# Performance work log

Hardware: AMD Instinct MI355X
Metric: run time of the kernel (lower is better)

## Reference

```python
import jax, jax.numpy as jnp
import numpy as np

B, S, D, L, V, H, FF = 128, 256, 512, 4, 96, 8, 512
DH = D // H
EPS = 1e-3  # keras BatchNormalization default epsilon


def setup_inputs() -> dict:
    key = jax.random.key(0)
    ks = jax.random.split(key, 12)
    s = 0.02
    inp = {
        "sequence": jax.random.randint(ks[0], (B, S), 0, V),
        "pos_encodings": jax.random.normal(ks[1], (S, D), jnp.float32) * s,
        "embed": jax.random.normal(ks[2], (V, D), jnp.float32) * s,
        "Wq": jax.random.normal(ks[3], (L, D, D), jnp.float32) * s,
        "bq": jnp.zeros((L, D), jnp.float32),
        "Wk": jax.random.normal(ks[4], (L, D, D), jnp.float32) * s,
        "bk": jnp.zeros((L, D), jnp.float32),
        "Wv": jax.random.normal(ks[5], (L, D, D), jnp.float32) * s,
        "bv": jnp.zeros((L, D), jnp.float32),
        "Wo": jax.random.normal(ks[6], (L, D, D), jnp.float32) * s,
        "bo": jnp.zeros((L, D), jnp.float32),
        "gamma1": jnp.ones((L, D), jnp.float32),
        "beta1": jnp.zeros((L, D), jnp.float32),
        "W1": jax.random.normal(ks[7], (L, D, FF), jnp.float32) * s,
        "b1": jnp.zeros((L, FF), jnp.float32),
        "W2": jax.random.normal(ks[8], (L, FF, D), jnp.float32) * s,
        "b2": jnp.zeros((L, D), jnp.float32),
        "gamma2": jnp.ones((L, D), jnp.float32),
        "beta2": jnp.zeros((L, D), jnp.float32),
    }
    return inp


def _batchnorm(h, g, b):
    # training-mode BN over (batch, seq) per feature, eps=1e-3
    mu = jnp.mean(h, axis=(0, 1), keepdims=True)
    var = jnp.mean(jnp.square(h - mu), axis=(0, 1), keepdims=True)
    return (h - mu) * jax.lax.rsqrt(var + EPS) * g + b


def _encoder(sequence, pos_encodings, embed, layer_params):
    x = embed[sequence] + pos_encodings[None]  # [B,S,D]

    def layer(h, p):
        wq, bq_, wk, bk_, wv, bv_, wo, bo_, g1, be1, w1, bb1, w2, bb2, g2, be2 = p
        b_, s_, d_ = h.shape
        q = (h @ wq + bq_).reshape(b_, s_, H, DH)
        k = (h @ wk + bk_).reshape(b_, s_, H, DH)
        v = (h @ wv + bv_).reshape(b_, s_, H, DH)
        scores = jnp.einsum('bqhd,bkhd->bhqk', q, k) / jnp.sqrt(jnp.float32(DH))
        attn = jnp.einsum('bhqk,bkhd->bqhd', jax.nn.softmax(scores, axis=-1), v)
        attn = attn.reshape(b_, s_, d_) @ wo + bo_
        h = _batchnorm(h + attn, g1, be1)
        ffn = jax.nn.relu(h @ w1 + bb1) @ w2 + bb2
        h = _batchnorm(h + ffn, g2, be2)
        return h, None

    out, _ = jax.lax.scan(layer, x, layer_params)
    return out


def reference(sequence, pos_encodings, embed, Wq, bq, Wk, bk, Wv, bv, Wo, bo,
              gamma1, beta1, W1, b1, W2, b2, gamma2, beta2):
    layer_params = (Wq, bq, Wk, bk, Wv, bv, Wo, bo,
                    gamma1, beta1, W1, b1, W2, b2, gamma2, beta2)
    return _encoder(sequence, pos_encodings, embed, layer_params)
```

## Files before the change

### kernel.cpp

```cpp
#include <hip/hip_runtime.h>

#define B_   128
#define S_   256
#define D_   512
#define L_   4
#define H_   8
#define DH_  64
#define FF_  512
#define M_   32768
#define EPS_ 1e-3f

typedef unsigned short u16;
typedef unsigned int   u32;
typedef __bf16 bf16_8 __attribute__((ext_vector_type(8)));
typedef float  f32_4  __attribute__((ext_vector_type(4)));

__device__ __forceinline__ float bf2f(u16 u) {
  union { u32 i; float f; } x; x.i = ((u32)u) << 16; return x.f;
}
__device__ __forceinline__ u16 f2bf(float f) {
  union { float f; u32 i; } x; x.f = f;
  u32 r = x.i + 0x7fffu + ((x.i >> 16) & 1u);
  return (u16)(r >> 16);
}
__device__ __forceinline__ void async_cp16(const void* g, void* l) {
  __builtin_amdgcn_global_load_lds(
      (const __attribute__((address_space(1))) void*)g,
      (__attribute__((address_space(3))) void*)l, 16, 0, 0);
}

__global__ __launch_bounds__(256) void k_embed(const int* __restrict__ seq,
    const float* __restrict__ pos, const float* __restrict__ emb,
    u16* __restrict__ h)
{
  int t = blockIdx.x * 256 + threadIdx.x;
  int row = t >> 6;
  int c = (t & 63) * 8;
  int s = row & (S_ - 1);
  int tok = seq[row];
  const float* ep = emb + (size_t)tok * D_ + c;
  const float* pp = pos + (size_t)s * D_ + c;
  float4 e0 = *(const float4*)ep;
  float4 e1 = *(const float4*)(ep + 4);
  float4 p0 = *(const float4*)pp;
  float4 p1 = *(const float4*)(pp + 4);
  u32 o[4];
  o[0] = (u32)f2bf(e0.x + p0.x) | ((u32)f2bf(e0.y + p0.y) << 16);
  o[1] = (u32)f2bf(e0.z + p0.z) | ((u32)f2bf(e0.w + p0.w) << 16);
  o[2] = (u32)f2bf(e1.x + p1.x) | ((u32)f2bf(e1.y + p1.y) << 16);
  o[3] = (u32)f2bf(e1.z + p1.z) | ((u32)f2bf(e1.w + p1.w) << 16);
  *(uint4*)&h[(size_t)row * D_ + c] = make_uint4(o[0], o[1], o[2], o[3]);
}

__global__ __launch_bounds__(256) void k_transpose(
    const float* __restrict__ Wq, const float* __restrict__ Wk, const float* __restrict__ Wv,
    const float* __restrict__ Wo, const float* __restrict__ W1, const float* __restrict__ W2,
    u16* __restrict__ Wt)
{
  __shared__ u16 tile[32][33];
  int mat = blockIdx.z;
  int layer = mat / 6, w = mat % 6;
  const float* src = (w == 0) ? Wq : (w == 1) ? Wk : (w == 2) ? Wv
                   : (w == 3) ? Wo : (w == 4) ? W1 : W2;
  src += (size_t)layer * (D_ * D_);
  u16* dst = Wt + (size_t)mat * (D_ * D_);
  int bx = blockIdx.x * 32;
  int by = blockIdx.y * 32;
  int tx = threadIdx.x & 31, ty = threadIdx.x >> 5;
#pragma unroll
  for (int i = 0; i < 32; i += 8)
    tile[ty + i][tx] = f2bf(src[(size_t)(by + ty + i) * D_ + bx + tx]);
  __syncthreads();
#pragma unroll
  for (int i = 0; i < 32; i += 8)
    dst[(size_t)(bx + ty + i) * D_ + by + tx] = tile[tx][ty + i];
}

__global__ __launch_bounds__(256) void k_packbias(const float* __restrict__ bq,
    const float* __restrict__ bk, const float* __restrict__ bv, float* __restrict__ dst)
{
  int t = blockIdx.x * 256 + threadIdx.x;
  int l = t / 1536, j = t - l * 1536;
  const float* src = (j < 512) ? bq : (j < 1024) ? bk : bv;
  dst[t] = src[l * 512 + (j & 511)];
}

__global__ __launch_bounds__(256) void k_gemm(
    const u16* __restrict__ A, const u16* __restrict__ Bt,
    const float* __restrict__ bias, const u16* __restrict__ resid,
    u16* __restrict__ outb, float* __restrict__ stats,
    int mode)
{
  __shared__ __align__(16) u16 smem[24576];
  u16* As = smem;
  u16* Bs = smem + 12288;
  int tid = threadIdx.x;
  int m0 = blockIdx.x * 128;
  int n0 = blockIdx.y * 128;
  int w = tid >> 6, lane = tid & 63;
  int wm = (w >> 1) * 64, wn = (w & 1) * 64;
  int fr = lane & 15, lk = lane >> 4;

  int srow = lane >> 2;
  int schunk = (lane & 3) ^ ((lane >> 4) & 3);
  const u16* Ag0 = A  + (size_t)(m0 + w * 32 + srow) * 512 + schunk * 8;
  const u16* Ag1 = Ag0 + (size_t)16 * 512;
  const u16* Bg0 = Bt + (size_t)(n0 + w * 32 + srow) * 512 + schunk * 8;
  const u16* Bg1 = Bg0 + (size_t)16 * 512;
  int off0 = (w * 32) * 32;
  int off1 = (w * 32 + 16) * 32;

  f32_4 acc[4][4] = {};
  int ach = (lk ^ ((fr >> 2) & 3)) * 8;

  async_cp16(Ag0, &As[off0]);
  async_cp16(Ag1, &As[off1]);
  async_cp16(Bg0, &Bs[off0]);
  async_cp16(Bg1, &Bs[off1]);
  async_cp16(Ag0 + 32, &As[4096 + off0]);
  async_cp16(Ag1 + 32, &As[4096 + off1]);
  async_cp16(Bg0 + 32, &Bs[4096 + off0]);
  async_cp16(Bg1 + 32, &Bs[4096 + off1]);

#pragma unroll
  for (int it = 0; it < 16; it++) {
    if (it < 15) asm volatile("s_waitcnt vmcnt(4)" ::: "memory");
    else         asm volatile("s_waitcnt vmcnt(0)" ::: "memory");
    __builtin_amdgcn_s_barrier();
    asm volatile("" ::: "memory");
    if (it < 14) {
      int kn = (it + 2) * 32;
      int pn = ((it + 2) % 3) * 4096;
      async_cp16(Ag0 + kn, &As[pn + off0]);
      async_cp16(Ag1 + kn, &As[pn + off1]);
      async_cp16(Bg0 + kn, &Bs[pn + off0]);
      async_cp16(Bg1 + kn, &Bs[pn + off1]);
    }
    const u16* Ab = &As[(it % 3) * 4096];
    const u16* Bb = &Bs[(it % 3) * 4096];
    bf16_8 afr[4], bfr[4];
#pragma unroll
    for (int i = 0; i < 4; i++) {
      afr[i] = *(const bf16_8*)&Ab[(wm + i * 16 + fr) * 32 + ach];
      bfr[i] = *(const bf16_8*)&Bb[(wn + i * 16 + fr) * 32 + ach];
    }
#pragma unroll
    for (int i = 0; i < 4; i++)
#pragma unroll
      for (int j = 0; j < 4; j++)
        acc[i][j] = __builtin_amdgcn_mfma_f32_16x16x32_bf16(afr[i], bfr[j], acc[i][j], 0, 0, 0);
  }

  __syncthreads();
  u16* Ct = smem;
  int rbase = lk * 4;
#pragma unroll
  for (int j = 0; j < 4; j++) {
    int colin = wn + j * 16 + fr;
    int colg  = n0 + colin;
    float bv = bias[colg];
    float csum = 0.f, csq = 0.f;
#pragma unroll
    for (int i = 0; i < 4; i++) {
      int rowl = wm + i * 16 + rbase;
#pragma unroll
      for (int r = 0; r < 4; r++) {
        float c = acc[i][j][r] + bv;
        if (mode == 1) c = fmaxf(c, 0.f);
        if (mode == 2) {
          c += bf2f(resid[(size_t)(m0 + rowl + r) * 512 + colg]);
          csum += c; csq = fmaf(c, c, csq);
        }
        int rw = rowl + r;
        Ct[rw * 128 + (((colin >> 3) ^ (rw & 15)) << 3) + (colin & 7)] = f2bf(c);
      }
    }
    if (mode == 2) {
      csum += __shfl_xor(csum, 16); csum += __shfl_xor(csum, 32);
      csq  += __shfl_xor(csq, 16);  csq  += __shfl_xor(csq, 32);
      if (lk == 0) {
        atomicAdd(&stats[colg], csum);
        atomicAdd(&stats[512 + colg], csq);
      }
    }
  }
  __syncthreads();

#pragma unroll
  for (int rd = 0; rd < 8; rd++) {
    int lrow = w * 32 + rd * 4 + (lane >> 4);
    int s = lane & 15;
    uint4 val = *(const uint4*)&Ct[lrow * 128 + s * 8];
    int chunk = s ^ (lrow & 15);
    int grow = m0 + lrow;
    if (mode == 3) {
      int colg = n0 + chunk * 8;
      int cc = colg & 511;
      size_t idx = (size_t)(colg >> 9) * ((size_t)M_ * D_)
                 + ((size_t)((grow >> 8) * 8 + (cc >> 6)) * 256 + (grow & 255)) * 64 + (cc & 63);
      *(uint4*)&outb[idx] = val;
    } else {
      *(uint4*)&outb[(size_t)grow * 512 + n0 + chunk * 8] = val;
    }
  }
}

__global__ __launch_bounds__(256) void k_attn(
    const u16* __restrict__ q, const u16* __restrict__ k,
    const u16* __restrict__ v, u16* __restrict__ attn)
{
  __shared__ u16 Vt[64 * 256];
  __shared__ u16 Pm[4][16 * 64];
  int tid = threadIdx.x;
  int h = blockIdx.x & 7, b = blockIdx.x >> 3;
  size_t hb = (size_t)(b * 8 + h) * (256 * 64);
  int w = tid >> 6, lane = tid & 63;

  {
    int kp = tid & 127;
    int o  = tid >> 7;
    const u16* vp = v + hb + (size_t)(2 * kp) * 64 + o * 32;
    union { uint4 u[4]; u16 s[32]; } r0, r1;
#pragma unroll
    for (int i = 0; i < 4; i++) {
      r0.u[i] = *(const uint4*)(vp + i * 8);
      r1.u[i] = *(const uint4*)(vp + 64 + i * 8);
    }
#pragma unroll
    for (int d = 0; d < 32; d++) {
      int da = o * 32 + d;
      u32 val = (u32)r0.s[d] | ((u32)r1.s[d] << 16);
      int idx = da * 256 + ((((kp >> 2) ^ (da & 31)) << 3)) + ((2 * kp) & 7);
      *(u32*)&Vt[idx] = val;
    }
  }
  __syncthreads();

  int fr = lane & 15;
  int lk = lane >> 4;
  int rbase = lk * 4;
  const u16* kb = k + hb;

#pragma unroll 1
  for (int qt = 0; qt < 4; qt++) {
    int q0 = qt * 64 + w * 16;

    f32_4 accS[16];
    const u16* qbase = q + hb + (size_t)(q0 + fr) * 64 + lk * 8;
    bf16_8 af0 = *(const bf16_8*)(qbase);
    bf16_8 af1 = *(const bf16_8*)(qbase + 32);
#pragma unroll
    for (int j = 0; j < 16; j++) {
      const u16* kr = kb + (size_t)(j * 16 + fr) * 64;
      bf16_8 bf0 = *(const bf16_8*)(kr + lk * 8);
      bf16_8 bf1 = *(const bf16_8*)(kr + 32 + lk * 8);
      f32_4 z = {};
      z = __builtin_amdgcn_mfma_f32_16x16x32_bf16(af0, bf0, z, 0, 0, 0);
      accS[j] = __builtin_amdgcn_mfma_f32_16x16x32_bf16(af1, bf1, z, 0, 0, 0);
    }

    float l[4];
#pragma unroll
    for (int r = 0; r < 4; r++) {
      float m = accS[0][r];
#pragma unroll
      for (int j = 1; j < 16; j++) m = fmaxf(m, accS[j][r]);
      m = fmaxf(m, __shfl_xor(m, 1));
      m = fmaxf(m, __shfl_xor(m, 2));
      m = fmaxf(m, __shfl_xor(m, 4));
      m = fmaxf(m, __shfl_xor(m, 8));
      float s = 0.f;
#pragma unroll
      for (int j = 0; j < 16; j++) {
        float p = __expf((accS[j][r] - m) * 0.125f);
        accS[j][r] = p;
        s += p;
      }
      s += __shfl_xor(s, 1);
      s += __shfl_xor(s, 2);
      s += __shfl_xor(s, 4);
      s += __shfl_xor(s, 8);
      l[r] = s;
    }

    f32_4 accO[4] = {};
#pragma unroll
    for (int hs = 0; hs < 4; hs++) {
#pragma unroll
      for (int j4 = 0; j4 < 4; j4++) {
        int col = j4 * 16 + fr;
        int ch = col >> 3, cl = col & 7;
#pragma unroll
        for (int r = 0; r < 4; r++) {
          int row = rbase + r;
          Pm[w][row * 64 + ((ch ^ (row & 7)) << 3) + cl] = f2bf(accS[hs * 4 + j4][r]);
        }
      }
#pragma unroll
      for (int kk = 0; kk < 2; kk++) {
        bf16_8 pa = *(const bf16_8*)&Pm[w][fr * 64 + (((kk * 4 + lk) ^ (fr & 7)) << 3)];
#pragma unroll
        for (int jd = 0; jd < 4; jd++) {
          int brow = jd * 16 + fr;
          int ck = hs * 8 + kk * 4 + lk;
          bf16_8 vb = *(const bf16_8*)&Vt[brow * 256 + ((ck ^ (brow & 31)) << 3)];
          accO[jd] = __builtin_amdgcn_mfma_f32_16x16x32_bf16(pa, vb, accO[jd], 0, 0, 0);
        }
      }
    }

    float linv[4];
#pragma unroll
    for (int r = 0; r < 4; r++) linv[r] = 1.f / l[r];
    size_t orow0 = (size_t)(b * S_ + q0 + rbase);
#pragma unroll
    for (int jd = 0; jd < 4; jd++) {
      int col = h * DH_ + jd * 16 + fr;
#pragma unroll
      for (int r = 0; r < 4; r++)
        attn[(orow0 + r) * D_ + col] = f2bf(accO[jd][r] * linv[r]);
    }
  }
}

__global__ __launch_bounds__(256) void k_zero(float* p, int n) {
  int t = blockIdx.x * 256 + threadIdx.x;
  if (t < n) p[t] = 0.f;
}

__global__ __launch_bounds__(256) void k_bnapply(const u16* __restrict__ P,
    const float* __restrict__ stats, const float* __restrict__ gamma,
    const float* __restrict__ beta, u16* __restrict__ outb, float* __restrict__ outf)
{
  size_t t8 = ((size_t)blockIdx.x * 256 + threadIdx.x) * 8;
  int f = (int)(t8 & 511);
  const float inv = 1.f / 32768.f;
  float sc[8], sh[8];
#pragma unroll
  for (int i = 0; i < 8; i++) {
    float mu = stats[f + i] * inv;
    float var = stats[512 + f + i] * inv - mu * mu;
    sc[i] = gamma[f + i] * rsqrtf(var + EPS_);
    sh[i] = beta[f + i] - mu * sc[i];
  }
  union { uint4 u; u16 s[8]; } pv;
  pv.u = *(const uint4*)&P[t8];
  float o[8];
#pragma unroll
  for (int i = 0; i < 8; i++) o[i] = bf2f(pv.s[i]) * sc[i] + sh[i];
  if (outf) {
    *(float4*)&outf[t8]     = make_float4(o[0], o[1], o[2], o[3]);
    *(float4*)&outf[t8 + 4] = make_float4(o[4], o[5], o[6], o[7]);
  } else {
    u32 u[4];
#pragma unroll
    for (int i = 0; i < 4; i++)
      u[i] = (u32)f2bf(o[2 * i]) | ((u32)f2bf(o[2 * i + 1]) << 16);
    *(uint4*)&outb[t8] = make_uint4(u[0], u[1], u[2], u[3]);
  }
}

extern "C" void kernel_launch(void* const* d_in, const int* in_sizes, int n_in,
                              void* d_out, int out_size, void* d_ws, size_t ws_size,
                              hipStream_t stream)
{
  const int*   seq = (const int*)d_in[0];
  const float* pos = (const float*)d_in[1];
  const float* emb = (const float*)d_in[2];
  const float* Wq  = (const float*)d_in[3];
  const float* bq  = (const float*)d_in[4];
  const float* Wk  = (const float*)d_in[5];
  const float* bk  = (const float*)d_in[6];
  const float* Wv  = (const float*)d_in[7];
  const float* bv  = (const float*)d_in[8];
  const float* Wo  = (const float*)d_in[9];
  const float* bo  = (const float*)d_in[10];
  const float* g1  = (const float*)d_in[11];
  const float* be1 = (const float*)d_in[12];
  const float* W1  = (const float*)d_in[13];
  const float* b1  = (const float*)d_in[14];
  const float* W2  = (const float*)d_in[15];
  const float* b2  = (const float*)d_in[16];
  const float* g2  = (const float*)d_in[17];
  const float* be2 = (const float*)d_in[18];

  char* ws = (char*)d_ws;
  const size_t SZH = (size_t)M_ * D_ * 2;
  u16* hb16 = (u16*)(ws);
  u16* qB   = (u16*)(ws + SZH);
  u16* kB   = (u16*)(ws + 2 * SZH);
  u16* vB   = (u16*)(ws + 3 * SZH);
  u16* aB   = (u16*)(ws + 4 * SZH);
  u16* PB   = (u16*)(ws + 2 * SZH);
  u16* tB   = qB;
  u16* Wt   = (u16*)(ws + 5 * SZH);
  float* stats = (float*)(ws + 5 * SZH + (size_t)24 * D_ * D_ * 2);
  float* bqkv  = stats + 8192;

  dim3 blk(256);
  k_zero<<<32, blk, 0, stream>>>(stats, 8192);
  k_packbias<<<24, blk, 0, stream>>>(bq, bk, bv, bqkv);
  k_transpose<<<dim3(16, 16, 24), blk, 0, stream>>>(Wq, Wk, Wv, Wo, W1, W2, Wt);
  k_embed<<<M_ * 64 / 256, blk, 0, stream>>>(seq, pos, emb, hb16);

  dim3 ggrid(M_ / 128, 512 / 128);
  dim3 qgrid(M_ / 128, 1536 / 128);
  for (int l = 0; l < L_; l++) {
    const u16* wtqkv = Wt + (size_t)(l * 6 + 0) * D_ * D_;
    const u16* wto = Wt + (size_t)(l * 6 + 3) * D_ * D_;
    const u16* wt1 = Wt + (size_t)(l * 6 + 4) * D_ * D_;
    const u16* wt2 = Wt + (size_t)(l * 6 + 5) * D_ * D_;
    float* st = stats + l * 2048;

    k_gemm<<<qgrid, blk, 0, stream>>>(hb16, wtqkv, bqkv + l * 1536, nullptr, qB, nullptr, 3);
    k_attn<<<B_ * H_, blk, 0, stream>>>(qB, kB, vB, aB);
    k_gemm<<<ggrid, blk, 0, stream>>>(aB, wto, bo + l * D_, hb16, PB, st, 2);
    k_bnapply<<<8192, blk, 0, stream>>>(PB, st, g1 + l * D_, be1 + l * D_, hb16, nullptr);
    k_gemm<<<ggrid, blk, 0, stream>>>(hb16, wt1, b1 + l * FF_, nullptr, tB, nullptr, 1);
    k_gemm<<<ggrid, blk, 0, stream>>>(tB, wt2, b2 + l * D_, hb16, PB, st + 1024, 2);
    if (l == L_ - 1)
      k_bnapply<<<8192, blk, 0, stream>>>(PB, st + 1024, g2 + l * D_, be2 + l * D_, nullptr, (float*)d_out);
    else
      k_bnapply<<<8192, blk, 0, stream>>>(PB, st + 1024, g2 + l * D_, be2 + l * D_, hb16, nullptr);
  }
}
```

Baseline: 1.561 ms.

## Recompute attention scores in two passes and swap GEMM grid order

The attention kernel no longer keeps all 16 score tiles in registers. A first pass computes QK^T only to get the row max, and a second pass recomputes the scores chunk by chunk, exponentiating and feeding P·V straight away. This cuts register pressure to allow more waves per CU, at the cost of computing QK^T twice. Separately, the GEMM grid now puts the N tiles on blockIdx.x, so blocks that share the same A rows launch next to each other and can reuse them in L2.

Measured after the change: 1.681 ms. 1.08x slower.

```diff
diff --git a/kernel.cpp b/kernel.cpp
--- a/kernel.cpp
+++ b/kernel.cpp
@@ -95,8 +95,8 @@
   u16* As = smem;
   u16* Bs = smem + 12288;
   int tid = threadIdx.x;
-  int m0 = blockIdx.x * 128;
-  int n0 = blockIdx.y * 128;
+  int m0 = blockIdx.y * 128;
+  int n0 = blockIdx.x * 128;
   int w = tid >> 6, lane = tid & 63;
   int wm = (w >> 1) * 64, wn = (w & 1) * 64;
   int fr = lane & 15, lk = lane >> 4;
@@ -244,74 +244,90 @@
 #pragma unroll 1
   for (int qt = 0; qt < 4; qt++) {
     int q0 = qt * 64 + w * 16;
-
-    f32_4 accS[16];
     const u16* qbase = q + hb + (size_t)(q0 + fr) * 64 + lk * 8;
     bf16_8 af0 = *(const bf16_8*)(qbase);
     bf16_8 af1 = *(const bf16_8*)(qbase + 32);
-#pragma unroll
+
+    float mrow[4] = {-1e30f, -1e30f, -1e30f, -1e30f};
+#pragma unroll 4
     for (int j = 0; j < 16; j++) {
       const u16* kr = kb + (size_t)(j * 16 + fr) * 64;
       bf16_8 bf0 = *(const bf16_8*)(kr + lk * 8);
       bf16_8 bf1 = *(const bf16_8*)(kr + 32 + lk * 8);
       f32_4 z = {};
       z = __builtin_amdgcn_mfma_f32_16x16x32_bf16(af0, bf0, z, 0, 0, 0);
-      accS[j] = __builtin_amdgcn_mfma_f32_16x16x32_bf16(af1, bf1, z, 0, 0, 0);
-    }
-
-    float l[4];
+      z = __builtin_amdgcn_mfma_f32_16x16x32_bf16(af1, bf1, z, 0, 0, 0);
+      mrow[0] = fmaxf(mrow[0], z[0]);
+      mrow[1] = fmaxf(mrow[1], z[1]);
+      mrow[2] = fmaxf(mrow[2], z[2]);
+      mrow[3] = fmaxf(mrow[3], z[3]);
+    }
 #pragma unroll
     for (int r = 0; r < 4; r++) {
-      float m = accS[0][r];
-#pragma unroll
-      for (int j = 1; j < 16; j++) m = fmaxf(m, accS[j][r]);
+      float m = mrow[r];
       m = fmaxf(m, __shfl_xor(m, 1));
       m = fmaxf(m, __shfl_xor(m, 2));
       m = fmaxf(m, __shfl_xor(m, 4));
       m = fmaxf(m, __shfl_xor(m, 8));
-      float s = 0.f;
-#pragma unroll
-      for (int j = 0; j < 16; j++) {
-        float p = __expf((accS[j][r] - m) * 0.125f);
-        accS[j][r] = p;
-        s += p;
-      }
+      mrow[r] = m;
+    }
+
+    float lrow[4] = {0.f, 0.f, 0.f, 0.f};
+    f32_4 accO[4] = {};
+#pragma unroll 1
+    for (int qq = 0; qq < 4; qq++) {
+      f32_4 accS4[4];
+#pragma unroll
+      for (int j4 = 0; j4 < 4; j4++) {
+        const u16* kr = kb + (size_t)((qq * 4 + j4) * 16 + fr) * 64;
+        bf16_8 bf0 = *(const bf16_8*)(kr + lk * 8);
+        bf16_8 bf1 = *(const bf16_8*)(kr + 32 + lk * 8);
+        f32_4 z = {};
+        z = __builtin_amdgcn_mfma_f32_16x16x32_bf16(af0, bf0, z, 0, 0, 0);
+        accS4[j4] = __builtin_amdgcn_mfma_f32_16x16x32_bf16(af1, bf1, z, 0, 0, 0);
+      }
+#pragma unroll
+      for (int r = 0; r < 4; r++) {
+#pragma unroll
+        for (int j4 = 0; j4 < 4; j4++) {
+          float p = __expf((accS4[j4][r] - mrow[r]) * 0.125f);
+          accS4[j4][r] = p;
+          lrow[r] += p;
+        }
+      }
+#pragma unroll
+      for (int j4 = 0; j4 < 4; j4++) {
+        int col = j4 * 16 + fr;
+        int ch = col >> 3, cl = col & 7;
+#pragma unroll
+        for (int r = 0; r < 4; r++) {
+          int row = rbase + r;
+          Pm[w][row * 64 + ((ch ^ (row & 7)) << 3) + cl] = f2bf(accS4[j4][r]);
+        }
+      }
+#pragma unroll
+      for (int kk = 0; kk < 2; kk++) {
+        bf16_8 pa = *(const bf16_8*)&Pm[w][fr * 64 + (((kk * 4 + lk) ^ (fr & 7)) << 3)];
+#pragma unroll
+        for (int jd = 0; jd < 4; jd++) {
+          int brow = jd * 16 + fr;
+          int ck = qq * 8 + kk * 4 + lk;
+          bf16_8 vb = *(const bf16_8*)&Vt[brow * 256 + ((ck ^ (brow & 31)) << 3)];
+          accO[jd] = __builtin_amdgcn_mfma_f32_16x16x32_bf16(pa, vb, accO[jd], 0, 0, 0);
+        }
+      }
+    }
+
+    float linv[4];
+#pragma unroll
+    for (int r = 0; r < 4; r++) {
+      float s = lrow[r];
       s += __shfl_xor(s, 1);
       s += __shfl_xor(s, 2);
       s += __shfl_xor(s, 4);
       s += __shfl_xor(s, 8);
-      l[r] = s;
-    }
-
-    f32_4 accO[4] = {};
-#pragma unroll
-    for (int hs = 0; hs < 4; hs++) {
-#pragma unroll
-      for (int j4 = 0; j4 < 4; j4++) {
-        int col = j4 * 16 + fr;
-        int ch = col >> 3, cl = col & 7;
-#pragma unroll
-        for (int r = 0; r < 4; r++) {
-          int row = rbase + r;
-          Pm[w][row * 64 + ((ch ^ (row & 7)) << 3) + cl] = f2bf(accS[hs * 4 + j4][r]);
-        }
-      }
-#pragma unroll
-      for (int kk = 0; kk < 2; kk++) {
-        bf16_8 pa = *(const bf16_8*)&Pm[w][fr * 64 + (((kk * 4 + lk) ^ (fr & 7)) << 3)];
-#pragma unroll
-        for (int jd = 0; jd < 4; jd++) {
-          int brow = jd * 16 + fr;
-          int ck = hs * 8 + kk * 4 + lk;
-          bf16_8 vb = *(const bf16_8*)&Vt[brow * 256 + ((ck ^ (brow & 31)) << 3)];
-          accO[jd] = __builtin_amdgcn_mfma_f32_16x16x32_bf16(pa, vb, accO[jd], 0, 0, 0);
-        }
-      }
-    }
-
-    float linv[4];
-#pragma unroll
-    for (int r = 0; r < 4; r++) linv[r] = 1.f / l[r];
+      linv[r] = 1.f / s;
+    }
     size_t orow0 = (size_t)(b * S_ + q0 + rbase);
 #pragma unroll
     for (int jd = 0; jd < 4; jd++) {
@@ -403,8 +419,8 @@
   k_transpose<<<dim3(16, 16, 24), blk, 0, stream>>>(Wq, Wk, Wv, Wo, W1, W2, Wt);
   k_embed<<<M_ * 64 / 256, blk, 0, stream>>>(seq, pos, emb, hb16);
 
-  dim3 ggrid(M_ / 128, 512 / 128);
-  dim3 qgrid(M_ / 128, 1536 / 128);
+  dim3 ggrid(512 / 128, M_ / 128);
+  dim3 qgrid(1536 / 128, M_ / 128);
   for (int l = 0; l < L_; l++) {
     const u16* wtqkv = Wt + (size_t)(l * 6 + 0) * D_ * D_;
     const u16* wto = Wt + (size_t)(l * 6 + 3) * D_ * D_;
```
